# Performance work log

Measured on AMD Instinct MI355X. Metric: run time of the kernel, lower is better.

## Reference

```python
import jax, jax.numpy as jnp
import numpy as np

# ---- model dims (match init_kwargs) ----
BATCH, SEQ, DM = 2, 256, 768
EXPAND, HD, NST = 2, 64, 64
DI = EXPAND * DM            # 1536 d_inner
NH = DI // HD               # 24 heads
R, G = 2, 1                 # mimo_rank, ngroups
SPLIT = NST // 2            # rope_fraction=0.5 -> 32 rotated state dims
NA = SPLIT // 2             # 16 rope angles
AFLOOR, EPS = 1e-4, 1e-5
DINP = 2 * DI + 2 * NST * G * R + 3 * NH + NA  # 3416


def setup_inputs() -> dict:
    key = jax.random.key(0)
    ks = jax.random.split(key, 10)
    def n(k, shp, s=1.0):
        return jax.random.normal(k, shp, jnp.float32) * s
    u = n(ks[0], (BATCH, SEQ, DM))
    in_proj_w = n(ks[1], (DINP, DM), 0.02)
    dt_bias = n(ks[2], (NH,), 0.5)
    B_bias = jnp.ones((NH, R, NST), jnp.float32) + n(ks[3], (NH, R, NST), 0.02)
    C_bias = jnp.ones((NH, R, NST), jnp.float32) + n(ks[4], (NH, R, NST), 0.02)
    B_norm_w = jnp.ones((NST,), jnp.float32)
    C_norm_w = jnp.ones((NST,), jnp.float32)
    mimo_x = jnp.ones((NH, R, HD), jnp.float32) / R + n(ks[5], (NH, R, HD), 0.02)
    mimo_o = jnp.ones((NH, R, HD), jnp.float32) / R + n(ks[6], (NH, R, HD), 0.02)
    D = jnp.ones((NH,), jnp.float32)
    out_proj_w = n(ks[7], (DM, DI), 0.02)
    return dict(u=u, in_proj_w=in_proj_w, dt_bias=dt_bias, B_bias=B_bias,
                C_bias=C_bias, B_norm_w=B_norm_w, C_norm_w=C_norm_w,
                mimo_x=mimo_x, mimo_o=mimo_o, D=D, out_proj_w=out_proj_w)


def _rms(x, w):
    return x * jax.lax.rsqrt(jnp.mean(x * x, -1, keepdims=True) + EPS) * w


def _rope(x, theta):
    # x: (b,l,r,h,n); theta: (b,l,h,NA). Rotate first SPLIT dims in consecutive pairs.
    b, l, r, h, n = x.shape
    xr = x[..., :SPLIT].reshape(b, l, r, h, NA, 2)
    c = jnp.cos(theta)[:, :, None]            # (b,l,1,h,NA)
    s = jnp.sin(theta)[:, :, None]
    x0, x1 = xr[..., 0], xr[..., 1]
    rot = jnp.stack([x0 * c - x1 * s, x0 * s + x1 * c], -1).reshape(b, l, r, h, SPLIT)
    return jnp.concatenate([rot, x[..., SPLIT:]], -1)


def _forward(u, in_proj_w, dt_bias, B_bias, C_bias, B_norm_w, C_norm_w,
             mimo_x, mimo_o, D, out_proj_w):
    b, l, _ = u.shape
    proj = u @ in_proj_w.T                                    # (b,l,DINP)
    sp = np.cumsum([DI, DI, NST * G * R, NST * G * R, NH, NH, NH])
    z, x, Bm, Cm, dd_dt, dd_A, trap, ang = jnp.split(proj, sp, axis=-1)
    z = z.reshape(b, l, NH, HD)
    x = x.reshape(b, l, NH, HD)
    Bm = Bm.reshape(b, l, R, G, NST)[:, :, :, 0]              # g=1 -> (b,l,r,n)
    Cm = Cm.reshape(b, l, R, G, NST)[:, :, :, 0]
    A = jnp.minimum(-jax.nn.softplus(dd_A), -AFLOOR)          # (b,l,h)
    DT = jax.nn.softplus(dd_dt + dt_bias)                     # (b,l,h)
    at = jnp.exp(A * DT)                                      # decay per step
    lam = jax.nn.sigmoid(trap)                                # trapezoid blend
    Bm = _rms(Bm, B_norm_w)
    Cm = _rms(Cm, C_norm_w)
    # per-head multiplicative bias (B_bias/C_bias init to ones -> scale) : (b,l,r,h,n)
    Bh = Bm[:, :, :, None, :] * B_bias.transpose(1, 0, 2)
    Ch = Cm[:, :, :, None, :] * C_bias.transpose(1, 0, 2)
    # data-dependent rotary: cumulative angle theta_t = sum_{s<=t} dt_s * angles_s
    theta = jnp.cumsum(DT[..., None] * ang[:, :, None, :], axis=1)  # (b,l,h,NA)
    Bh = _rope(Bh, theta)
    Ch = _rope(Ch, theta)
    mv = mimo_x.transpose(1, 0, 2)                            # (r,h,p)
    mo = mimo_o.transpose(1, 0, 2)                            # (r,h,p)

    def step(carry, inp):
        S, Bp, vp = carry                                      # S:(b,r,h,p,n)
        Bt, Ct, vt, att, dtt, lamt, zt = inp
        f = jnp.einsum('brhp,brhn->brhpn', vt[:, None] * mv, Bt)
        fp = jnp.einsum('brhp,brhn->brhpn', vp[:, None] * mv, Bp)
        a5 = att[:, None, :, None, None]
        d5 = dtt[:, None, :, None, None]
        l5 = lamt[:, None, :, None, None]
        S = a5 * S + d5 * (l5 * f + (1.0 - l5) * a5 * fp)      # trapezoidal update
        y = jnp.einsum('brhn,brhpn->brhp', Ct, S)
        y = jnp.einsum('brhp,rhp->bhp', y, mo) + D[None, :, None] * vt
        y = y * jax.nn.silu(zt)                                # gated output
        return (S, Bt, vt), y

    S0 = jnp.zeros((b, R, NH, HD, NST), jnp.float32)
    B0 = jnp.zeros((b, R, NH, NST), jnp.float32)
    v0 = jnp.zeros((b, NH, HD), jnp.float32)
    inps = (jnp.moveaxis(Bh, 1, 0), jnp.moveaxis(Ch, 1, 0), jnp.moveaxis(x, 1, 0),
            jnp.moveaxis(at, 1, 0), jnp.moveaxis(DT, 1, 0), jnp.moveaxis(lam, 1, 0),
            jnp.moveaxis(z, 1, 0))
    _, ys = jax.lax.scan(step, (S0, B0, v0), inps)             # ys:(l,b,h,p)
    y = jnp.moveaxis(ys, 0, 1).reshape(b, l, DI)
    return y @ out_proj_w.T                                    # (b,l,DM)


def reference(u, in_proj_w, dt_bias, B_bias, C_bias, B_norm_w, C_norm_w,
              mimo_x, mimo_o, D, out_proj_w):
    return _forward(u, in_proj_w, dt_bias, B_bias, C_bias, B_norm_w, C_norm_w,
                    mimo_x, mimo_o, D, out_proj_w)
```

## Files before the change

kernel.cpp:

```cpp
#include <hip/hip_runtime.h>
#include <hip/hip_bf16.h>
#include <math.h>

typedef __bf16 bf16x8 __attribute__((ext_vector_type(8)));
typedef float  f32x4  __attribute__((ext_vector_type(4)));

#define BATCH 2
#define SEQ   256
#define DMODL 768
#define DIEXP 1536
#define NHEAD 24
#define HDIM  64
#define NSTATE 64
#define RRANK 2
#define NANG  16
#define HALFSPLIT 32
#define DINP  3416
#define DINP_PAD 3456
#define AFLOOR 1e-4f
#define EPSV   1e-5f

__device__ __forceinline__ float softplusf(float x) {
    if (x > 20.f) return x;
    return log1pf(expf(x));
}
__device__ __forceinline__ float sigmoidf_(float x) {
    return 1.f / (1.f + __expf(-x));
}
__device__ __forceinline__ ushort f2bf(float f) {
    uint u = __float_as_uint(f);
    uint r = (u + 0x7FFFu + ((u >> 16) & 1u)) >> 16;
    return (ushort)r;
}
__device__ __forceinline__ float bf2f(ushort x) {
    uint u = ((uint)x) << 16;
    return __uint_as_float(u);
}

__global__ __launch_bounds__(256) void gemm1(const float* __restrict__ A,
        const float* __restrict__ W, ushort* __restrict__ ZT, ushort* __restrict__ XT,
        ushort* __restrict__ BC, float* __restrict__ DTA) {
    const int bm = blockIdx.y * 64, bn = blockIdx.x * 64;
    const int tid = threadIdx.x;
    const int wv = tid >> 6, lane = tid & 63;
    const int wr = (wv >> 1) * 32, wc = (wv & 1) * 32;
    __shared__ ushort As[2][64 * 64];
    __shared__ ushort Bs[2][64 * 64];
    __shared__ ushort Ts[64][72];
    const int srow = tid >> 4, sc4 = tid & 15;
    const int NT = DMODL >> 6;
    float4 ra[4], rw[4];

    auto load_tile = [&](int t) {
        const int k0 = t * 64;
        #pragma unroll
        for (int p = 0; p < 4; ++p)
            ra[p] = *(const float4*)(A + (size_t)(bm + p * 16 + srow) * DMODL + k0 + sc4 * 4);
        #pragma unroll
        for (int p = 0; p < 4; ++p) {
            int r = p * 16 + srow;
            rw[p] = (bn + r < DINP)
                  ? *(const float4*)(W + (size_t)(bn + r) * DMODL + k0 + sc4 * 4)
                  : (float4){0.f, 0.f, 0.f, 0.f};
        }
    };
    auto write_tile = [&](int buf) {
        #pragma unroll
        for (int p = 0; p < 4; ++p) {
            int r = p * 16 + srow;
            int byt = (sc4 * 8) ^ ((r & 7) << 4);
            ushort4 h;
            h.x = f2bf(ra[p].x); h.y = f2bf(ra[p].y);
            h.z = f2bf(ra[p].z); h.w = f2bf(ra[p].w);
            *(ushort4*)(&As[buf][r * 64 + (byt >> 1)]) = h;
        }
        #pragma unroll
        for (int p = 0; p < 4; ++p) {
            int r = p * 16 + srow;
            int byt = (sc4 * 8) ^ ((r & 7) << 4);
            ushort4 h;
            h.x = f2bf(rw[p].x); h.y = f2bf(rw[p].y);
            h.z = f2bf(rw[p].z); h.w = f2bf(rw[p].w);
            *(ushort4*)(&Bs[buf][r * 64 + (byt >> 1)]) = h;
        }
    };

    f32x4 acc[2][2];
    #pragma unroll
    for (int m = 0; m < 2; ++m)
        #pragma unroll
        for (int n = 0; n < 2; ++n) acc[m][n] = (f32x4){0.f, 0.f, 0.f, 0.f};
    const int fr = lane & 15, fk = (lane >> 4) * 16;

    auto compute = [&](int buf) {
        #pragma unroll
        for (int kk = 0; kk < 2; ++kk) {
            bf16x8 af[2], bff[2];
            #pragma unroll
            for (int m = 0; m < 2; ++m) {
                int r = wr + m * 16 + fr;
                int byt = (kk * 64 + fk) ^ ((r & 7) << 4);
                af[m] = *(const bf16x8*)(&As[buf][r * 64 + (byt >> 1)]);
            }
            #pragma unroll
            for (int n = 0; n < 2; ++n) {
                int r = wc + n * 16 + fr;
                int byt = (kk * 64 + fk) ^ ((r & 7) << 4);
                bff[n] = *(const bf16x8*)(&Bs[buf][r * 64 + (byt >> 1)]);
            }
            #pragma unroll
            for (int m = 0; m < 2; ++m)
                #pragma unroll
                for (int n = 0; n < 2; ++n)
                    acc[m][n] = __builtin_amdgcn_mfma_f32_16x16x32_bf16(af[m], bff[n], acc[m][n], 0, 0, 0);
        }
    };

    load_tile(0);
    write_tile(0);
    __syncthreads();
    for (int t = 0; t < NT; ++t) {
        if (t + 1 < NT) load_tile(t + 1);
        compute(t & 1);
        if (t + 1 < NT) write_tile((t + 1) & 1);
        __syncthreads();
    }

    const int r0 = bm + wr + (lane >> 4) * 4;
    if (bn >= 3328) {
        #pragma unroll
        for (int n = 0; n < 2; ++n) {
            int col = bn + wc + n * 16 + fr;
            #pragma unroll
            for (int m = 0; m < 2; ++m)
                #pragma unroll
                for (int r = 0; r < 4; ++r)
                    DTA[(size_t)(col - 3328) * 512 + r0 + m * 16 + r] = acc[m][n][r];
        }
        return;
    }
    #pragma unroll
    for (int m = 0; m < 2; ++m)
        #pragma unroll
        for (int n = 0; n < 2; ++n)
            #pragma unroll
            for (int r = 0; r < 4; ++r)
                Ts[wr + m * 16 + (lane >> 4) * 4 + r][wc + n * 16 + fr] =
                    f2bf(acc[m][n][r]);
    __syncthreads();
    if (bn < 3072) {
        const bool isX = bn >= 1536;
        const int hh = (bn - (isX ? 1536 : 0)) >> 6;
        const int bb = bm >> 8, l0 = bm & 255;
        ushort* dst = (isX ? XT : ZT);
        const int p = tid >> 2, t0 = (tid & 3) * 16;
        ushort* o = dst + ((size_t)(bb * NHEAD + hh) * HDIM + p) * SEQ + l0 + t0;
        #pragma unroll
        for (int k = 0; k < 16; ++k) o[k] = Ts[t0 + k][p];
    } else {
        const int c0 = bn - 3072;
        const int rr = tid >> 2, cs = (tid & 3) * 16;
        ushort* o = BC + (size_t)(bm + rr) * 256 + c0 + cs;
        #pragma unroll
        for (int k = 0; k < 16; ++k) o[k] = Ts[rr][cs + k];
    }
}

__global__ __launch_bounds__(256) void gemm2(const ushort* __restrict__ A,
        const float* __restrict__ W, float* __restrict__ Part) {
    const int bm = blockIdx.y * 64, bn = blockIdx.x * 64, ks = blockIdx.z;
    const int kbase = ks * 384;
    const int tid = threadIdx.x;
    const int wv = tid >> 6, lane = tid & 63;
    const int wr = (wv >> 1) * 32, wc = (wv & 1) * 32;
    __shared__ ushort As[2][64 * 64];
    __shared__ ushort Bs[2][64 * 64];
    const int srow = tid >> 4, sc4 = tid & 15;
    const int arow = tid >> 3, acol = (tid & 7) * 8;
    const int NT = 6;
    uint4 ra[2];
    float4 rw[4];

    auto load_tile = [&](int t) {
        const int k0 = kbase + t * 64;
        #pragma unroll
        for (int p = 0; p < 2; ++p)
            ra[p] = *(const uint4*)(A + (size_t)(bm + p * 32 + arow) * DIEXP + k0 + acol);
        #pragma unroll
        for (int p = 0; p < 4; ++p)
            rw[p] = *(const float4*)(W + (size_t)(bn + p * 16 + srow) * DIEXP + k0 + sc4 * 4);
    };
    auto write_tile = [&](int buf) {
        #pragma unroll
        for (int p = 0; p < 2; ++p) {
            int r = p * 32 + arow;
            int byt = (acol * 2) ^ ((r & 7) << 4);
            *(uint4*)(&As[buf][r * 64 + (byt >> 1)]) = ra[p];
        }
        #pragma unroll
        for (int p = 0; p < 4; ++p) {
            int r = p * 16 + srow;
            int byt = (sc4 * 8) ^ ((r & 7) << 4);
            ushort4 h;
            h.x = f2bf(rw[p].x); h.y = f2bf(rw[p].y);
            h.z = f2bf(rw[p].z); h.w = f2bf(rw[p].w);
            *(ushort4*)(&Bs[buf][r * 64 + (byt >> 1)]) = h;
        }
    };

    f32x4 acc[2][2];
    #pragma unroll
    for (int m = 0; m < 2; ++m)
        #pragma unroll
        for (int n = 0; n < 2; ++n) acc[m][n] = (f32x4){0.f, 0.f, 0.f, 0.f};
    const int fr = lane & 15, fk = (lane >> 4) * 16;

    auto compute = [&](int buf) {
        #pragma unroll
        for (int kk = 0; kk < 2; ++kk) {
            bf16x8 af[2], bff[2];
            #pragma unroll
            for (int m = 0; m < 2; ++m) {
                int r = wr + m * 16 + fr;
                int byt = (kk * 64 + fk) ^ ((r & 7) << 4);
                af[m] = *(const bf16x8*)(&As[buf][r * 64 + (byt >> 1)]);
            }
            #pragma unroll
            for (int n = 0; n < 2; ++n) {
                int r = wc + n * 16 + fr;
                int byt = (kk * 64 + fk) ^ ((r & 7) << 4);
                bff[n] = *(const bf16x8*)(&Bs[buf][r * 64 + (byt >> 1)]);
            }
            #pragma unroll
            for (int m = 0; m < 2; ++m)
                #pragma unroll
                for (int n = 0; n < 2; ++n)
                    acc[m][n] = __builtin_amdgcn_mfma_f32_16x16x32_bf16(af[m], bff[n], acc[m][n], 0, 0, 0);
        }
    };

    load_tile(0);
    write_tile(0);
    __syncthreads();
    for (int t = 0; t < NT; ++t) {
        if (t + 1 < NT) load_tile(t + 1);
        compute(t & 1);
        if (t + 1 < NT) write_tile((t + 1) & 1);
        __syncthreads();
    }

    const int r0 = bm + wr + (lane >> 4) * 4;
    float* P = Part + (size_t)ks * 512 * DMODL;
    #pragma unroll
    for (int n = 0; n < 2; ++n) {
        int col = bn + wc + n * 16 + fr;
        #pragma unroll
        for (int m = 0; m < 2; ++m)
            #pragma unroll
            for (int r = 0; r < 4; ++r)
                P[(size_t)(r0 + m * 16 + r) * DMODL + col] = acc[m][n][r];
    }
}

__global__ void reduce4(const float* __restrict__ Part, float* __restrict__ out) {
    const int i = blockIdx.x * 256 + threadIdx.x;
    const float4* p4 = (const float4*)Part;
    float4 a = p4[i];
    float4 b = p4[i + 98304];
    float4 c = p4[i + 196608];
    float4 d = p4[i + 294912];
    float4 r;
    r.x = a.x + b.x + c.x + d.x;
    r.y = a.y + b.y + c.y + d.y;
    r.z = a.z + b.z + c.z + d.z;
    r.w = a.w + b.w + c.w + d.w;
    ((float4*)out)[i] = r;
}

__global__ __launch_bounds__(256) void scan_kernel(const float* __restrict__ DTA,
        const float* __restrict__ dt_bias, float* __restrict__ DTv,
        float* __restrict__ lamv, float* __restrict__ Pc, float* __restrict__ theta) {
    const int bh = blockIdx.x;
    const int b = bh / NHEAD, h = bh % NHEAD;
    const int tid = threadIdx.x;
    __shared__ float mm[SEQ][18];
    const int l = tid;
    const int gl = b * SEQ + l;
    float DT  = softplusf(DTA[(size_t)h * 512 + gl] + dt_bias[h]);
    float Asp = fmaxf(softplusf(DTA[(size_t)(24 + h) * 512 + gl]), AFLOOR);
    float la  = -Asp * DT;
    float lam = sigmoidf_(DTA[(size_t)(48 + h) * 512 + gl]);
    DTv[bh * SEQ + l] = DT;
    lamv[bh * SEQ + l] = lam;
    #pragma unroll
    for (int i = 0; i < NANG; ++i) mm[l][i] = DT * DTA[(size_t)(72 + i) * 512 + gl];
    mm[l][16] = la;
    __syncthreads();
    const int wv = tid >> 6, lane = tid & 63;
    for (int ch = wv; ch < 17; ch += 4) {
        float carry = 0.f;
        for (int seg = 0; seg < 4; ++seg) {
            float v = mm[seg * 64 + lane][ch];
            #pragma unroll
            for (int off = 1; off < 64; off <<= 1) {
                float t = __shfl_up(v, off);
                if (lane >= off) v += t;
            }
            v += carry;
            carry = __shfl(v, 63);
            int ll = seg * 64 + lane;
            if (ch < 16)
                theta[((size_t)(b * SEQ + ll) * NHEAD + h) * NANG + ch] = v;
            else
                Pc[bh * SEQ + ll] = v;
        }
    }
}

__global__ __launch_bounds__(256) void prep3(const ushort* __restrict__ BC,
        const float* __restrict__ Bbias, const float* __restrict__ Cbias,
        const float* __restrict__ Bnw, const float* __restrict__ Cnw,
        const float* __restrict__ theta,
        ushort* __restrict__ Bh, ushort* __restrict__ Ch) {
    int bl = blockIdx.x;
    int b = bl / SEQ, l = bl % SEQ;
    int tid = threadIdx.x;
    __shared__ float sB[RRANK][NSTATE], sC[RRANK][NSTATE], scale[4];
    __shared__ float thl[NHEAD * NANG];
    const ushort* row = BC + (size_t)bl * 256;
    if (tid < 128) {
        int r = tid / 64, n = tid % 64;
        sB[r][n] = bf2f(row[r * 64 + n]);
    } else {
        int t2 = tid - 128;
        int r = t2 / 64, n = t2 % 64;
        sC[r][n] = bf2f(row[128 + r * 64 + n]);
    }
    for (int k = tid; k < NHEAD * NANG; k += 256)
        thl[k] = theta[(size_t)bl * NHEAD * NANG + k];
    __syncthreads();
    int g = tid / 64, lane = tid % 64;
    float v = (g < 2) ? sB[g][lane] : sC[g - 2][lane];
    float ss = v * v;
    #pragma unroll
    for (int off = 32; off; off >>= 1) ss += __shfl_xor(ss, off);
    if (lane == 0) scale[g] = rsqrtf(ss / NSTATE + EPSV);
    __syncthreads();
    float scB[2] = {scale[0], scale[1]};
    float scC[2] = {scale[2], scale[3]};
    for (int idx = tid; idx < RRANK * NHEAD * NSTATE; idx += 256) {
        int n = idx % NSTATE;
        int h = (idx / NSTATE) % NHEAD;
        int r = idx / (NSTATE * NHEAD);
        float outB, outC;
        if (n < HALFSPLIT) {
            int i = n >> 1;
            int n0 = i * 2, n1 = n0 + 1;
            float th = thl[h * NANG + i];
            float c = cosf(th), s = sinf(th);
            float b0 = sB[r][n0] * scB[r] * Bnw[n0] * Bbias[(h * RRANK + r) * NSTATE + n0];
            float b1 = sB[r][n1] * scB[r] * Bnw[n1] * Bbias[(h * RRANK + r) * NSTATE + n1];
            float c0 = sC[r][n0] * scC[r] * Cnw[n0] * Cbias[(h * RRANK + r) * NSTATE + n0];
            float c1 = sC[r][n1] * scC[r] * Cnw[n1] * Cbias[(h * RRANK + r) * NSTATE + n1];
            outB = (n & 1) ? (b0 * s + b1 * c) : (b0 * c - b1 * s);
            outC = (n & 1) ? (c0 * s + c1 * c) : (c0 * c - c1 * s);
        } else {
            outB = sB[r][n] * scB[r] * Bnw[n] * Bbias[(h * RRANK + r) * NSTATE + n];
            outC = sC[r][n] * scC[r] * Cnw[n] * Cbias[(h * RRANK + r) * NSTATE + n];
        }
        size_t o = ((size_t)((b * RRANK + r) * NHEAD + h) * SEQ + l) * NSTATE + n;
        Bh[o] = f2bf(outB);
        Ch[o] = f2bf(outC);
    }
}

__global__ __launch_bounds__(256) void att2(const ushort* __restrict__ Bh,
        const ushort* __restrict__ Ch, const ushort* __restrict__ XT,
        const ushort* __restrict__ ZT, const float* __restrict__ Pc,
        const float* __restrict__ DTv, const float* __restrict__ lamv,
        const float* __restrict__ mimo_x, const float* __restrict__ mimo_o,
        const float* __restrict__ Dvec, ushort* __restrict__ Yc) {
    const int bh = blockIdx.x, tt = blockIdx.y;
    const int b = bh / NHEAD, h = bh % NHEAD;
    const int tid = threadIdx.x, wv = tid >> 6, lane = tid & 63;
    __shared__ float Pl[SEQ], u1s[SEQ], u2s[SEQ];
    __shared__ ushort Pld[2][4][16][72];
    for (int t = tid; t < SEQ; t += 256) {
        Pl[t]  = Pc[bh * SEQ + t];
        u1s[t] = DTv[bh * SEQ + t] * lamv[bh * SEQ + t];
        u2s[t] = (t + 1 < SEQ) ? DTv[bh * SEQ + t + 1] * (1.f - lamv[bh * SEQ + t + 1]) : 0.f;
    }
    __syncthreads();
    const int r16 = lane & 15, kg = (lane >> 4) * 8;
    const int trow = tt * 64 + wv * 16;
    const int tr0 = trow + (lane >> 4) * 4;
    const int brh0 = (b * RRANK + 0) * NHEAD + h;
    const int brh1 = (b * RRANK + 1) * NHEAD + h;
    bf16x8 ca[2][2];
    {
        const ushort* cp0 = Ch + ((size_t)brh0 * SEQ + trow + r16) * NSTATE + kg;
        const ushort* cp1 = Ch + ((size_t)brh1 * SEQ + trow + r16) * NSTATE + kg;
        ca[0][0] = *(const bf16x8*)cp0;  ca[0][1] = *(const bf16x8*)(cp0 + 32);
        ca[1][0] = *(const bf16x8*)cp1;  ca[1][1] = *(const bf16x8*)(cp1 + 32);
    }
    f32x4 yacc[2][4];
    #pragma unroll
    for (int r2 = 0; r2 < 2; ++r2)
        #pragma unroll
        for (int pf = 0; pf < 4; ++pf) yacc[r2][pf] = (f32x4){0.f, 0.f, 0.f, 0.f};
    float Pt[4];
    #pragma unroll
    for (int r = 0; r < 4; ++r) Pt[r] = Pl[tr0 + r];
    const float Dh = Dvec[h];

    for (int jt = 0; jt <= tt; ++jt) {
        bf16x8 xf[4][2];
        #pragma unroll
        for (int pf = 0; pf < 4; ++pf) {
            const ushort* xp = XT + ((size_t)bh * HDIM + pf * 16 + r16) * SEQ + jt * 64 + kg;
            xf[pf][0] = *(const bf16x8*)xp;
            xf[pf][1] = *(const bf16x8*)(xp + 32);
        }
        f32x4 g[2][4];
        #pragma unroll
        for (int r2 = 0; r2 < 2; ++r2) {
            const size_t bbase = (size_t)(r2 ? brh1 : brh0) * SEQ;
            #pragma unroll
            for (int nf = 0; nf < 4; ++nf) {
                const ushort* bp = Bh + (bbase + jt * 64 + nf * 16 + r16) * NSTATE + kg;
                bf16x8 b0 = *(const bf16x8*)bp;
                bf16x8 b1 = *(const bf16x8*)(bp + 32);
                f32x4 gg = (f32x4){0.f, 0.f, 0.f, 0.f};
                gg = __builtin_amdgcn_mfma_f32_16x16x32_bf16(ca[r2][0], b0, gg, 0, 0, 0);
                gg = __builtin_amdgcn_mfma_f32_16x16x32_bf16(ca[r2][1], b1, gg, 0, 0, 0);
                g[r2][nf] = gg;
            }
        }
        float w[4][4];
        #pragma unroll
        for (int nf = 0; nf < 4; ++nf) {
            const int j = jt * 64 + nf * 16 + r16;
            const float Pj = Pl[j], v1 = u1s[j], v2 = u2s[j];
            #pragma unroll
            for (int r = 0; r < 4; ++r) {
                const int t = tr0 + r;
                w[nf][r] = (j <= t) ? __expf(Pt[r] - Pj) * (v1 + ((j < t) ? v2 : 0.f)) : 0.f;
            }
        }
        #pragma unroll
        for (int r2 = 0; r2 < 2; ++r2)
            #pragma unroll
            for (int nf = 0; nf < 4; ++nf)
                #pragma unroll
                for (int r = 0; r < 4; ++r)
                    Pld[r2][wv][(lane >> 4) * 4 + r][nf * 16 + r16] = f2bf(g[r2][nf][r] * w[nf][r]);
        #pragma unroll
        for (int r2 = 0; r2 < 2; ++r2) {
            bf16x8 pa0 = *(const bf16x8*)&Pld[r2][wv][r16][kg];
            bf16x8 pa1 = *(const bf16x8*)&Pld[r2][wv][r16][32 + kg];
            #pragma unroll
            for (int pf = 0; pf < 4; ++pf) {
                yacc[r2][pf] = __builtin_amdgcn_mfma_f32_16x16x32_bf16(pa0, xf[pf][0], yacc[r2][pf], 0, 0, 0);
                yacc[r2][pf] = __builtin_amdgcn_mfma_f32_16x16x32_bf16(pa1, xf[pf][1], yacc[r2][pf], 0, 0, 0);
            }
        }
    }
    #pragma unroll
    for (int pf = 0; pf < 4; ++pf) {
        const int p = pf * 16 + r16;
        const float mm0 = mimo_x[(h * RRANK + 0) * HDIM + p] * mimo_o[(h * RRANK + 0) * HDIM + p];
        const float mm1 = mimo_x[(h * RRANK + 1) * HDIM + p] * mimo_o[(h * RRANK + 1) * HDIM + p];
        ushort4 xv4 = *(const ushort4*)&XT[((size_t)bh * HDIM + p) * SEQ + tr0];
        ushort4 zv4 = *(const ushort4*)&ZT[((size_t)bh * HDIM + p) * SEQ + tr0];
        const ushort* xvp = (const ushort*)&xv4;
        const ushort* zvp = (const ushort*)&zv4;
        #pragma unroll
        for (int r = 0; r < 4; ++r) {
            const int t = tr0 + r;
            float xv = bf2f(xvp[r]);
            float zv = bf2f(zvp[r]);
            float y = yacc[0][pf][r] * mm0 + yacc[1][pf][r] * mm1 + Dh * xv;
            y *= zv * sigmoidf_(zv);
            Yc[(size_t)(b * SEQ + t) * DIEXP + h * HDIM + p] = f2bf(y);
        }
    }
}

extern "C" void kernel_launch(void* const* d_in, const int* in_sizes, int n_in,
                              void* d_out, int out_size, void* d_ws, size_t ws_size,
                              hipStream_t stream) {
    const float* u        = (const float*)d_in[0];
    const float* in_w     = (const float*)d_in[1];
    const float* dt_bias  = (const float*)d_in[2];
    const float* B_bias   = (const float*)d_in[3];
    const float* C_bias   = (const float*)d_in[4];
    const float* B_norm_w = (const float*)d_in[5];
    const float* C_norm_w = (const float*)d_in[6];
    const float* mimo_x   = (const float*)d_in[7];
    const float* mimo_o   = (const float*)d_in[8];
    const float* Dvec     = (const float*)d_in[9];
    const float* out_w    = (const float*)d_in[10];
    float* out = (float*)d_out;

    float* ws = (float*)d_ws;
    ushort* ZT    = (ushort*)(ws);
    ushort* XT    = (ushort*)(ws + 393216);
    ushort* BC    = (ushort*)(ws + 786432);
    float*  DTA   = ws + 851968;
    ushort* Bh_bf = (ushort*)(ws + 917504);
    ushort* Ch_bf = (ushort*)(ws + 1703936);
    float*  theta = ws + 2490368;
    float*  Pc    = ws + 2686976;
    float*  DTv   = ws + 2699264;
    float*  lamv  = ws + 2711552;
    ushort* Yc_bf = (ushort*)(ws + 2723840);
    float*  Part  = ws + 3117056;

    gemm1<<<dim3(DINP_PAD / 64, 8), 256, 0, stream>>>(u, in_w, ZT, XT, BC, DTA);
    scan_kernel<<<BATCH * NHEAD, 256, 0, stream>>>(DTA, dt_bias, DTv, lamv, Pc, theta);
    prep3<<<BATCH * SEQ, 256, 0, stream>>>(BC, B_bias, C_bias, B_norm_w, C_norm_w,
                                           theta, Bh_bf, Ch_bf);
    att2<<<dim3(BATCH * NHEAD, 4), 256, 0, stream>>>(Bh_bf, Ch_bf, XT, ZT, Pc, DTv,
                                                     lamv, mimo_x, mimo_o, Dvec, Yc_bf);
    gemm2<<<dim3(DMODL / 64, 8, 4), 256, 0, stream>>>(Yc_bf, out_w, Part);
    reduce4<<<384, 256, 0, stream>>>(Part, out);
}
```

Before: 66.34 us.

## Fuse scan with B/C prep and replace split-K reduce with atomics

Merges the cumulative-sum scan kernel and the per-token B/C normalisation+RoPE kernel into one per-(batch,head) kernel that keeps theta in shared memory instead of round-tripping through global memory. That kernel also zeroes the output buffer, so the split-K out-projection GEMM can atomically add into it and the separate partials buffer and reduce kernel are dropped. This removes two launches and the theta and partial-sum traffic. In exchange the prep work is spread over only 48 blocks, float atomics make the summation order nondeterministic, and __sincosf is less accurate than sinf/cosf.

Result: slower. 101.6 us (+53.2%).

```diff
diff --git a/kernel.cpp b/kernel.cpp
--- a/kernel.cpp
+++ b/kernel.cpp
@@ -166,124 +166,23 @@
     }
 }
 
-__global__ __launch_bounds__(256) void gemm2(const ushort* __restrict__ A,
-        const float* __restrict__ W, float* __restrict__ Part) {
-    const int bm = blockIdx.y * 64, bn = blockIdx.x * 64, ks = blockIdx.z;
-    const int kbase = ks * 384;
-    const int tid = threadIdx.x;
-    const int wv = tid >> 6, lane = tid & 63;
-    const int wr = (wv >> 1) * 32, wc = (wv & 1) * 32;
-    __shared__ ushort As[2][64 * 64];
-    __shared__ ushort Bs[2][64 * 64];
-    const int srow = tid >> 4, sc4 = tid & 15;
-    const int arow = tid >> 3, acol = (tid & 7) * 8;
-    const int NT = 6;
-    uint4 ra[2];
-    float4 rw[4];
-
-    auto load_tile = [&](int t) {
-        const int k0 = kbase + t * 64;
-        #pragma unroll
-        for (int p = 0; p < 2; ++p)
-            ra[p] = *(const uint4*)(A + (size_t)(bm + p * 32 + arow) * DIEXP + k0 + acol);
-        #pragma unroll
-        for (int p = 0; p < 4; ++p)
-            rw[p] = *(const float4*)(W + (size_t)(bn + p * 16 + srow) * DIEXP + k0 + sc4 * 4);
-    };
-    auto write_tile = [&](int buf) {
-        #pragma unroll
-        for (int p = 0; p < 2; ++p) {
-            int r = p * 32 + arow;
-            int byt = (acol * 2) ^ ((r & 7) << 4);
-            *(uint4*)(&As[buf][r * 64 + (byt >> 1)]) = ra[p];
-        }
-        #pragma unroll
-        for (int p = 0; p < 4; ++p) {
-            int r = p * 16 + srow;
-            int byt = (sc4 * 8) ^ ((r & 7) << 4);
-            ushort4 h;
-            h.x = f2bf(rw[p].x); h.y = f2bf(rw[p].y);
-            h.z = f2bf(rw[p].z); h.w = f2bf(rw[p].w);
-            *(ushort4*)(&Bs[buf][r * 64 + (byt >> 1)]) = h;
-        }
-    };
-
-    f32x4 acc[2][2];
-    #pragma unroll
-    for (int m = 0; m < 2; ++m)
-        #pragma unroll
-        for (int n = 0; n < 2; ++n) acc[m][n] = (f32x4){0.f, 0.f, 0.f, 0.f};
-    const int fr = lane & 15, fk = (lane >> 4) * 16;
-
-    auto compute = [&](int buf) {
-        #pragma unroll
-        for (int kk = 0; kk < 2; ++kk) {
-            bf16x8 af[2], bff[2];
-            #pragma unroll
-            for (int m = 0; m < 2; ++m) {
-                int r = wr + m * 16 + fr;
-                int byt = (kk * 64 + fk) ^ ((r & 7) << 4);
-                af[m] = *(const bf16x8*)(&As[buf][r * 64 + (byt >> 1)]);
-            }
-            #pragma unroll
-            for (int n = 0; n < 2; ++n) {
-                int r = wc + n * 16 + fr;
-                int byt = (kk * 64 + fk) ^ ((r & 7) << 4);
-                bff[n] = *(const bf16x8*)(&Bs[buf][r * 64 + (byt >> 1)]);
-            }
-            #pragma unroll
-            for (int m = 0; m < 2; ++m)
-                #pragma unroll
-                for (int n = 0; n < 2; ++n)
-                    acc[m][n] = __builtin_amdgcn_mfma_f32_16x16x32_bf16(af[m], bff[n], acc[m][n], 0, 0, 0);
-        }
-    };
-
-    load_tile(0);
-    write_tile(0);
-    __syncthreads();
-    for (int t = 0; t < NT; ++t) {
-        if (t + 1 < NT) load_tile(t + 1);
-        compute(t & 1);
-        if (t + 1 < NT) write_tile((t + 1) & 1);
-        __syncthreads();
-    }
-
-    const int r0 = bm + wr + (lane >> 4) * 4;
-    float* P = Part + (size_t)ks * 512 * DMODL;
-    #pragma unroll
-    for (int n = 0; n < 2; ++n) {
-        int col = bn + wc + n * 16 + fr;
-        #pragma unroll
-        for (int m = 0; m < 2; ++m)
-            #pragma unroll
-            for (int r = 0; r < 4; ++r)
-                P[(size_t)(r0 + m * 16 + r) * DMODL + col] = acc[m][n][r];
-    }
-}
-
-__global__ void reduce4(const float* __restrict__ Part, float* __restrict__ out) {
-    const int i = blockIdx.x * 256 + threadIdx.x;
-    const float4* p4 = (const float4*)Part;
-    float4 a = p4[i];
-    float4 b = p4[i + 98304];
-    float4 c = p4[i + 196608];
-    float4 d = p4[i + 294912];
-    float4 r;
-    r.x = a.x + b.x + c.x + d.x;
-    r.y = a.y + b.y + c.y + d.y;
-    r.z = a.z + b.z + c.z + d.z;
-    r.w = a.w + b.w + c.w + d.w;
-    ((float4*)out)[i] = r;
-}
-
-__global__ __launch_bounds__(256) void scan_kernel(const float* __restrict__ DTA,
-        const float* __restrict__ dt_bias, float* __restrict__ DTv,
-        float* __restrict__ lamv, float* __restrict__ Pc, float* __restrict__ theta) {
+__global__ __launch_bounds__(256) void scanprep(const float* __restrict__ DTA,
+        const ushort* __restrict__ BC, const float* __restrict__ dt_bias,
+        const float* __restrict__ Bbias, const float* __restrict__ Cbias,
+        const float* __restrict__ Bnw, const float* __restrict__ Cnw,
+        float* __restrict__ DTv, float* __restrict__ lamv, float* __restrict__ Pc,
+        ushort* __restrict__ Bh, ushort* __restrict__ Ch, float* __restrict__ outZ) {
     const int bh = blockIdx.x;
     const int b = bh / NHEAD, h = bh % NHEAD;
     const int tid = threadIdx.x;
+    {
+        float4* o4 = (float4*)outZ;
+        int base = bh * 2048 + tid;
+        #pragma unroll
+        for (int k = 0; k < 8; ++k) o4[base + k * 256] = (float4){0.f, 0.f, 0.f, 0.f};
+    }
     __shared__ float mm[SEQ][18];
+    __shared__ float thl[SEQ][NANG];
     const int l = tid;
     const int gl = b * SEQ + l;
     float DT  = softplusf(DTA[(size_t)h * 512 + gl] + dt_bias[h]);
@@ -310,67 +209,57 @@
             carry = __shfl(v, 63);
             int ll = seg * 64 + lane;
             if (ch < 16)
-                theta[((size_t)(b * SEQ + ll) * NHEAD + h) * NANG + ch] = v;
+                thl[ll][ch] = v;
             else
                 Pc[bh * SEQ + ll] = v;
         }
     }
-}
-
-__global__ __launch_bounds__(256) void prep3(const ushort* __restrict__ BC,
-        const float* __restrict__ Bbias, const float* __restrict__ Cbias,
-        const float* __restrict__ Bnw, const float* __restrict__ Cnw,
-        const float* __restrict__ theta,
-        ushort* __restrict__ Bh, ushort* __restrict__ Ch) {
-    int bl = blockIdx.x;
-    int b = bl / SEQ, l = bl % SEQ;
-    int tid = threadIdx.x;
-    __shared__ float sB[RRANK][NSTATE], sC[RRANK][NSTATE], scale[4];
-    __shared__ float thl[NHEAD * NANG];
-    const ushort* row = BC + (size_t)bl * 256;
-    if (tid < 128) {
-        int r = tid / 64, n = tid % 64;
-        sB[r][n] = bf2f(row[r * 64 + n]);
-    } else {
-        int t2 = tid - 128;
-        int r = t2 / 64, n = t2 % 64;
-        sC[r][n] = bf2f(row[128 + r * 64 + n]);
-    }
-    for (int k = tid; k < NHEAD * NANG; k += 256)
-        thl[k] = theta[(size_t)bl * NHEAD * NANG + k];
     __syncthreads();
-    int g = tid / 64, lane = tid % 64;
-    float v = (g < 2) ? sB[g][lane] : sC[g - 2][lane];
-    float ss = v * v;
-    #pragma unroll
-    for (int off = 32; off; off >>= 1) ss += __shfl_xor(ss, off);
-    if (lane == 0) scale[g] = rsqrtf(ss / NSTATE + EPSV);
-    __syncthreads();
-    float scB[2] = {scale[0], scale[1]};
-    float scC[2] = {scale[2], scale[3]};
-    for (int idx = tid; idx < RRANK * NHEAD * NSTATE; idx += 256) {
-        int n = idx % NSTATE;
-        int h = (idx / NSTATE) % NHEAD;
-        int r = idx / (NSTATE * NHEAD);
-        float outB, outC;
+    const int n = lane;
+    const float bw  = Bnw[n], cw = Cnw[n];
+    const float bb0 = Bbias[(h * RRANK + 0) * NSTATE + n];
+    const float bb1 = Bbias[(h * RRANK + 1) * NSTATE + n];
+    const float cb0 = Cbias[(h * RRANK + 0) * NSTATE + n];
+    const float cb1 = Cbias[(h * RRANK + 1) * NSTATE + n];
+    for (int ll = wv; ll < SEQ; ll += 4) {
+        const ushort* row = BC + (size_t)(b * SEQ + ll) * 256;
+        float vB0 = bf2f(row[n]);
+        float vB1 = bf2f(row[64 + n]);
+        float vC0 = bf2f(row[128 + n]);
+        float vC1 = bf2f(row[192 + n]);
+        float s0 = vB0 * vB0, s1 = vB1 * vB1, s2 = vC0 * vC0, s3 = vC1 * vC1;
+        #pragma unroll
+        for (int off = 32; off; off >>= 1) {
+            s0 += __shfl_xor(s0, off); s1 += __shfl_xor(s1, off);
+            s2 += __shfl_xor(s2, off); s3 += __shfl_xor(s3, off);
+        }
+        float b0 = vB0 * rsqrtf(s0 / 64.f + EPSV) * bw * bb0;
+        float b1 = vB1 * rsqrtf(s1 / 64.f + EPSV) * bw * bb1;
+        float c0 = vC0 * rsqrtf(s2 / 64.f + EPSV) * cw * cb0;
+        float c1 = vC1 * rsqrtf(s3 / 64.f + EPSV) * cw * cb1;
+        float pB0 = __shfl_xor(b0, 1), pB1 = __shfl_xor(b1, 1);
+        float pC0 = __shfl_xor(c0, 1), pC1 = __shfl_xor(c1, 1);
+        float outB0 = b0, outB1 = b1, outC0 = c0, outC1 = c1;
         if (n < HALFSPLIT) {
-            int i = n >> 1;
-            int n0 = i * 2, n1 = n0 + 1;
-            float th = thl[h * NANG + i];
-            float c = cosf(th), s = sinf(th);
-            float b0 = sB[r][n0] * scB[r] * Bnw[n0] * Bbias[(h * RRANK + r) * NSTATE + n0];
-            float b1 = sB[r][n1] * scB[r] * Bnw[n1] * Bbias[(h * RRANK + r) * NSTATE + n1];
-            float c0 = sC[r][n0] * scC[r] * Cnw[n0] * Cbias[(h * RRANK + r) * NSTATE + n0];
-            float c1 = sC[r][n1] * scC[r] * Cnw[n1] * Cbias[(h * RRANK + r) * NSTATE + n1];
-            outB = (n & 1) ? (b0 * s + b1 * c) : (b0 * c - b1 * s);
-            outC = (n & 1) ? (c0 * s + c1 * c) : (c0 * c - c1 * s);
-        } else {
-            outB = sB[r][n] * scB[r] * Bnw[n] * Bbias[(h * RRANK + r) * NSTATE + n];
-            outC = sC[r][n] * scC[r] * Cnw[n] * Cbias[(h * RRANK + r) * NSTATE + n];
-        }
-        size_t o = ((size_t)((b * RRANK + r) * NHEAD + h) * SEQ + l) * NSTATE + n;
-        Bh[o] = f2bf(outB);
-        Ch[o] = f2bf(outC);
+            float th = thl[ll][n >> 1];
+            float sth, cth;
+            __sincosf(th, &sth, &cth);
+            if ((n & 1) == 0) {
+                outB0 = b0 * cth - pB0 * sth;
+                outB1 = b1 * cth - pB1 * sth;
+                outC0 = c0 * cth - pC0 * sth;
+                outC1 = c1 * cth - pC1 * sth;
+            } else {
+                outB0 = pB0 * sth + b0 * cth;
+                outB1 = pB1 * sth + b1 * cth;
+                outC0 = pC0 * sth + c0 * cth;
+                outC1 = pC1 * sth + c1 * cth;
+            }
+        }
+        size_t o0 = ((size_t)((b * RRANK + 0) * NHEAD + h) * SEQ + ll) * NSTATE + n;
+        size_t o1 = ((size_t)((b * RRANK + 1) * NHEAD + h) * SEQ + ll) * NSTATE + n;
+        Bh[o0] = f2bf(outB0);  Bh[o1] = f2bf(outB1);
+        Ch[o0] = f2bf(outC0);  Ch[o1] = f2bf(outC1);
     }
 }
 
@@ -486,6 +375,101 @@
     }
 }
 
+__global__ __launch_bounds__(256) void gemm2(const ushort* __restrict__ A,
+        const float* __restrict__ W, float* __restrict__ out) {
+    const int bm = blockIdx.y * 64, bn = blockIdx.x * 64, ks = blockIdx.z;
+    const int kbase = ks * 384;
+    const int tid = threadIdx.x;
+    const int wv = tid >> 6, lane = tid & 63;
+    const int wr = (wv >> 1) * 32, wc = (wv & 1) * 32;
+    __shared__ ushort As[2][64 * 64];
+    __shared__ ushort Bs[2][64 * 64];
+    const int srow = tid >> 4, sc4 = tid & 15;
+    const int arow = tid >> 3, acol = (tid & 7) * 8;
+    const int NT = 6;
+    uint4 ra[2];
+    float4 rw[4];
+
+    auto load_tile = [&](int t) {
+        const int k0 = kbase + t * 64;
+        #pragma unroll
+        for (int p = 0; p < 2; ++p)
+            ra[p] = *(const uint4*)(A + (size_t)(bm + p * 32 + arow) * DIEXP + k0 + acol);
+        #pragma unroll
+        for (int p = 0; p < 4; ++p)
+            rw[p] = *(const float4*)(W + (size_t)(bn + p * 16 + srow) * DIEXP + k0 + sc4 * 4);
+    };
+    auto write_tile = [&](int buf) {
+        #pragma unroll
+        for (int p = 0; p < 2; ++p) {
+            int r = p * 32 + arow;
+            int byt = (acol * 2) ^ ((r & 7) << 4);
+            *(uint4*)(&As[buf][r * 64 + (byt >> 1)]) = ra[p];
+        }
+        #pragma unroll
+        for (int p = 0; p < 4; ++p) {
+            int r = p * 16 + srow;
+            int byt = (sc4 * 8) ^ ((r & 7) << 4);
+            ushort4 h;
+            h.x = f2bf(rw[p].x); h.y = f2bf(rw[p].y);
+            h.z = f2bf(rw[p].z); h.w = f2bf(rw[p].w);
+            *(ushort4*)(&Bs[buf][r * 64 + (byt >> 1)]) = h;
+        }
+    };
+
+    f32x4 acc[2][2];
+    #pragma unroll
+    for (int m = 0; m < 2; ++m)
+        #pragma unroll
+        for (int n = 0; n < 2; ++n) acc[m][n] = (f32x4){0.f, 0.f, 0.f, 0.f};
+    const int fr = lane & 15, fk = (lane >> 4) * 16;
+
+    auto compute = [&](int buf) {
+        #pragma unroll
+        for (int kk = 0; kk < 2; ++kk) {
+            bf16x8 af[2], bff[2];
+            #pragma unroll
+            for (int m = 0; m < 2; ++m) {
+                int r = wr + m * 16 + fr;
+                int byt = (kk * 64 + fk) ^ ((r & 7) << 4);
+                af[m] = *(const bf16x8*)(&As[buf][r * 64 + (byt >> 1)]);
+            }
+            #pragma unroll
+            for (int n = 0; n < 2; ++n) {
+                int r = wc + n * 16 + fr;
+                int byt = (kk * 64 + fk) ^ ((r & 7) << 4);
+                bff[n] = *(const bf16x8*)(&Bs[buf][r * 64 + (byt >> 1)]);
+            }
+            #pragma unroll
+            for (int m = 0; m < 2; ++m)
+                #pragma unroll
+                for (int n = 0; n < 2; ++n)
+                    acc[m][n] = __builtin_amdgcn_mfma_f32_16x16x32_bf16(af[m], bff[n], acc[m][n], 0, 0, 0);
+        }
+    };
+
+    load_tile(0);
+    write_tile(0);
+    __syncthreads();
+    for (int t = 0; t < NT; ++t) {
+        if (t + 1 < NT) load_tile(t + 1);
+        compute(t & 1);
+        if (t + 1 < NT) write_tile((t + 1) & 1);
+        __syncthreads();
+    }
+
+    const int r0 = bm + wr + (lane >> 4) * 4;
+    #pragma unroll
+    for (int n = 0; n < 2; ++n) {
+        int col = bn + wc + n * 16 + fr;
+        #pragma unroll
+        for (int m = 0; m < 2; ++m)
+            #pragma unroll
+            for (int r = 0; r < 4; ++r)
+                atomicAdd(&out[(size_t)(r0 + m * 16 + r) * DMODL + col], acc[m][n][r]);
+    }
+}
+
 extern "C" void kernel_launch(void* const* d_in, const int* in_sizes, int n_in,
                               void* d_out, int out_size, void* d_ws, size_t ws_size,
                               hipStream_t stream) {
@@ -509,19 +493,16 @@
     float*  DTA   = ws + 851968;
     ushort* Bh_bf = (ushort*)(ws + 917504);
     ushort* Ch_bf = (ushort*)(ws + 1703936);
-    float*  theta = ws + 2490368;
-    float*  Pc    = ws + 2686976;
-    float*  DTv   = ws + 2699264;
-    float*  lamv  = ws + 2711552;
-    ushort* Yc_bf = (ushort*)(ws + 2723840);
-    float*  Part  = ws + 3117056;
+    float*  Pc    = ws + 2490368;
+    float*  DTv   = ws + 2502656;
+    float*  lamv  = ws + 2514944;
+    ushort* Yc_bf = (ushort*)(ws + 2527232);
 
     gemm1<<<dim3(DINP_PAD / 64, 8), 256, 0, stream>>>(u, in_w, ZT, XT, BC, DTA);
-    scan_kernel<<<BATCH * NHEAD, 256, 0, stream>>>(DTA, dt_bias, DTv, lamv, Pc, theta);
-    prep3<<<BATCH * SEQ, 256, 0, stream>>>(BC, B_bias, C_bias, B_norm_w, C_norm_w,
-                                           theta, Bh_bf, Ch_bf);
+    scanprep<<<BATCH * NHEAD, 256, 0, stream>>>(DTA, BC, dt_bias, B_bias, C_bias,
+                                                B_norm_w, C_norm_w, DTv, lamv, Pc,
+                                                Bh_bf, Ch_bf, out);
     att2<<<dim3(BATCH * NHEAD, 4), 256, 0, stream>>>(Bh_bf, Ch_bf, XT, ZT, Pc, DTv,
                                                      lamv, mimo_x, mimo_o, Dvec, Yc_bf);
-    gemm2<<<dim3(DMODL / 64, 8, 4), 256, 0, stream>>>(Yc_bf, out_w, Part);
-    reduce4<<<384, 256, 0, stream>>>(Part, out);
-}
+    gemm2<<<dim3(DMODL / 64, 8, 4), 256, 0, stream>>>(Yc_bf, out_w, out);
+}
```

## Replace split-K partial buffer and reduce kernel with atomic accumulation into output

Applied to the files above, without the earlier changes.

The out-projection GEMM now atomically adds its four split-K partial results straight into the output instead of writing partials to workspace and launching a separate reduce kernel. The output is zeroed inside the scan kernel, which runs earlier in the stream, so no extra launch is needed. Separately, the rope cos/sin in prep3 now use the fast __sincosf intrinsic. This removes one launch and the round trip through the partial buffer. In exchange it adds atomic contention, a nondeterministic summation order and slightly lower sincos accuracy.

New measurement: 64.98 us, median of 2. -2.0%, faster.

```diff
diff --git a/kernel.cpp b/kernel.cpp
--- a/kernel.cpp
+++ b/kernel.cpp
@@ -166,123 +166,19 @@
     }
 }
 
-__global__ __launch_bounds__(256) void gemm2(const ushort* __restrict__ A,
-        const float* __restrict__ W, float* __restrict__ Part) {
-    const int bm = blockIdx.y * 64, bn = blockIdx.x * 64, ks = blockIdx.z;
-    const int kbase = ks * 384;
-    const int tid = threadIdx.x;
-    const int wv = tid >> 6, lane = tid & 63;
-    const int wr = (wv >> 1) * 32, wc = (wv & 1) * 32;
-    __shared__ ushort As[2][64 * 64];
-    __shared__ ushort Bs[2][64 * 64];
-    const int srow = tid >> 4, sc4 = tid & 15;
-    const int arow = tid >> 3, acol = (tid & 7) * 8;
-    const int NT = 6;
-    uint4 ra[2];
-    float4 rw[4];
-
-    auto load_tile = [&](int t) {
-        const int k0 = kbase + t * 64;
-        #pragma unroll
-        for (int p = 0; p < 2; ++p)
-            ra[p] = *(const uint4*)(A + (size_t)(bm + p * 32 + arow) * DIEXP + k0 + acol);
-        #pragma unroll
-        for (int p = 0; p < 4; ++p)
-            rw[p] = *(const float4*)(W + (size_t)(bn + p * 16 + srow) * DIEXP + k0 + sc4 * 4);
-    };
-    auto write_tile = [&](int buf) {
-        #pragma unroll
-        for (int p = 0; p < 2; ++p) {
-            int r = p * 32 + arow;
-            int byt = (acol * 2) ^ ((r & 7) << 4);
-            *(uint4*)(&As[buf][r * 64 + (byt >> 1)]) = ra[p];
-        }
-        #pragma unroll
-        for (int p = 0; p < 4; ++p) {
-            int r = p * 16 + srow;
-            int byt = (sc4 * 8) ^ ((r & 7) << 4);
-            ushort4 h;
-            h.x = f2bf(rw[p].x); h.y = f2bf(rw[p].y);
-            h.z = f2bf(rw[p].z); h.w = f2bf(rw[p].w);
-            *(ushort4*)(&Bs[buf][r * 64 + (byt >> 1)]) = h;
-        }
-    };
-
-    f32x4 acc[2][2];
-    #pragma unroll
-    for (int m = 0; m < 2; ++m)
-        #pragma unroll
-        for (int n = 0; n < 2; ++n) acc[m][n] = (f32x4){0.f, 0.f, 0.f, 0.f};
-    const int fr = lane & 15, fk = (lane >> 4) * 16;
-
-    auto compute = [&](int buf) {
-        #pragma unroll
-        for (int kk = 0; kk < 2; ++kk) {
-            bf16x8 af[2], bff[2];
-            #pragma unroll
-            for (int m = 0; m < 2; ++m) {
-                int r = wr + m * 16 + fr;
-                int byt = (kk * 64 + fk) ^ ((r & 7) << 4);
-                af[m] = *(const bf16x8*)(&As[buf][r * 64 + (byt >> 1)]);
-            }
-            #pragma unroll
-            for (int n = 0; n < 2; ++n) {
-                int r = wc + n * 16 + fr;
-                int byt = (kk * 64 + fk) ^ ((r & 7) << 4);
-                bff[n] = *(const bf16x8*)(&Bs[buf][r * 64 + (byt >> 1)]);
-            }
-            #pragma unroll
-            for (int m = 0; m < 2; ++m)
-                #pragma unroll
-                for (int n = 0; n < 2; ++n)
-                    acc[m][n] = __builtin_amdgcn_mfma_f32_16x16x32_bf16(af[m], bff[n], acc[m][n], 0, 0, 0);
-        }
-    };
-
-    load_tile(0);
-    write_tile(0);
-    __syncthreads();
-    for (int t = 0; t < NT; ++t) {
-        if (t + 1 < NT) load_tile(t + 1);
-        compute(t & 1);
-        if (t + 1 < NT) write_tile((t + 1) & 1);
-        __syncthreads();
-    }
-
-    const int r0 = bm + wr + (lane >> 4) * 4;
-    float* P = Part + (size_t)ks * 512 * DMODL;
-    #pragma unroll
-    for (int n = 0; n < 2; ++n) {
-        int col = bn + wc + n * 16 + fr;
-        #pragma unroll
-        for (int m = 0; m < 2; ++m)
-            #pragma unroll
-            for (int r = 0; r < 4; ++r)
-                P[(size_t)(r0 + m * 16 + r) * DMODL + col] = acc[m][n][r];
-    }
-}
-
-__global__ void reduce4(const float* __restrict__ Part, float* __restrict__ out) {
-    const int i = blockIdx.x * 256 + threadIdx.x;
-    const float4* p4 = (const float4*)Part;
-    float4 a = p4[i];
-    float4 b = p4[i + 98304];
-    float4 c = p4[i + 196608];
-    float4 d = p4[i + 294912];
-    float4 r;
-    r.x = a.x + b.x + c.x + d.x;
-    r.y = a.y + b.y + c.y + d.y;
-    r.z = a.z + b.z + c.z + d.z;
-    r.w = a.w + b.w + c.w + d.w;
-    ((float4*)out)[i] = r;
-}
-
 __global__ __launch_bounds__(256) void scan_kernel(const float* __restrict__ DTA,
         const float* __restrict__ dt_bias, float* __restrict__ DTv,
-        float* __restrict__ lamv, float* __restrict__ Pc, float* __restrict__ theta) {
+        float* __restrict__ lamv, float* __restrict__ Pc, float* __restrict__ theta,
+        float* __restrict__ outZ) {
     const int bh = blockIdx.x;
     const int b = bh / NHEAD, h = bh % NHEAD;
     const int tid = threadIdx.x;
+    {
+        float4* o4 = (float4*)outZ;
+        int base = bh * 2048 + tid;
+        #pragma unroll
+        for (int k = 0; k < 8; ++k) o4[base + k * 256] = (float4){0.f, 0.f, 0.f, 0.f};
+    }
     __shared__ float mm[SEQ][18];
     const int l = tid;
     const int gl = b * SEQ + l;
@@ -357,7 +253,8 @@
             int i = n >> 1;
             int n0 = i * 2, n1 = n0 + 1;
             float th = thl[h * NANG + i];
-            float c = cosf(th), s = sinf(th);
+            float c, s;
+            __sincosf(th, &s, &c);
             float b0 = sB[r][n0] * scB[r] * Bnw[n0] * Bbias[(h * RRANK + r) * NSTATE + n0];
             float b1 = sB[r][n1] * scB[r] * Bnw[n1] * Bbias[(h * RRANK + r) * NSTATE + n1];
             float c0 = sC[r][n0] * scC[r] * Cnw[n0] * Cbias[(h * RRANK + r) * NSTATE + n0];
@@ -486,6 +383,101 @@
     }
 }
 
+__global__ __launch_bounds__(256) void gemm2(const ushort* __restrict__ A,
+        const float* __restrict__ W, float* __restrict__ out) {
+    const int bm = blockIdx.y * 64, bn = blockIdx.x * 64, ks = blockIdx.z;
+    const int kbase = ks * 384;
+    const int tid = threadIdx.x;
+    const int wv = tid >> 6, lane = tid & 63;
+    const int wr = (wv >> 1) * 32, wc = (wv & 1) * 32;
+    __shared__ ushort As[2][64 * 64];
+    __shared__ ushort Bs[2][64 * 64];
+    const int srow = tid >> 4, sc4 = tid & 15;
+    const int arow = tid >> 3, acol = (tid & 7) * 8;
+    const int NT = 6;
+    uint4 ra[2];
+    float4 rw[4];
+
+    auto load_tile = [&](int t) {
+        const int k0 = kbase + t * 64;
+        #pragma unroll
+        for (int p = 0; p < 2; ++p)
+            ra[p] = *(const uint4*)(A + (size_t)(bm + p * 32 + arow) * DIEXP + k0 + acol);
+        #pragma unroll
+        for (int p = 0; p < 4; ++p)
+            rw[p] = *(const float4*)(W + (size_t)(bn + p * 16 + srow) * DIEXP + k0 + sc4 * 4);
+    };
+    auto write_tile = [&](int buf) {
+        #pragma unroll
+        for (int p = 0; p < 2; ++p) {
+            int r = p * 32 + arow;
+            int byt = (acol * 2) ^ ((r & 7) << 4);
+            *(uint4*)(&As[buf][r * 64 + (byt >> 1)]) = ra[p];
+        }
+        #pragma unroll
+        for (int p = 0; p < 4; ++p) {
+            int r = p * 16 + srow;
+            int byt = (sc4 * 8) ^ ((r & 7) << 4);
+            ushort4 h;
+            h.x = f2bf(rw[p].x); h.y = f2bf(rw[p].y);
+            h.z = f2bf(rw[p].z); h.w = f2bf(rw[p].w);
+            *(ushort4*)(&Bs[buf][r * 64 + (byt >> 1)]) = h;
+        }
+    };
+
+    f32x4 acc[2][2];
+    #pragma unroll
+    for (int m = 0; m < 2; ++m)
+        #pragma unroll
+        for (int n = 0; n < 2; ++n) acc[m][n] = (f32x4){0.f, 0.f, 0.f, 0.f};
+    const int fr = lane & 15, fk = (lane >> 4) * 16;
+
+    auto compute = [&](int buf) {
+        #pragma unroll
+        for (int kk = 0; kk < 2; ++kk) {
+            bf16x8 af[2], bff[2];
+            #pragma unroll
+            for (int m = 0; m < 2; ++m) {
+                int r = wr + m * 16 + fr;
+                int byt = (kk * 64 + fk) ^ ((r & 7) << 4);
+                af[m] = *(const bf16x8*)(&As[buf][r * 64 + (byt >> 1)]);
+            }
+            #pragma unroll
+            for (int n = 0; n < 2; ++n) {
+                int r = wc + n * 16 + fr;
+                int byt = (kk * 64 + fk) ^ ((r & 7) << 4);
+                bff[n] = *(const bf16x8*)(&Bs[buf][r * 64 + (byt >> 1)]);
+            }
+            #pragma unroll
+            for (int m = 0; m < 2; ++m)
+                #pragma unroll
+                for (int n = 0; n < 2; ++n)
+                    acc[m][n] = __builtin_amdgcn_mfma_f32_16x16x32_bf16(af[m], bff[n], acc[m][n], 0, 0, 0);
+        }
+    };
+
+    load_tile(0);
+    write_tile(0);
+    __syncthreads();
+    for (int t = 0; t < NT; ++t) {
+        if (t + 1 < NT) load_tile(t + 1);
+        compute(t & 1);
+        if (t + 1 < NT) write_tile((t + 1) & 1);
+        __syncthreads();
+    }
+
+    const int r0 = bm + wr + (lane >> 4) * 4;
+    #pragma unroll
+    for (int n = 0; n < 2; ++n) {
+        int col = bn + wc + n * 16 + fr;
+        #pragma unroll
+        for (int m = 0; m < 2; ++m)
+            #pragma unroll
+            for (int r = 0; r < 4; ++r)
+                atomicAdd(&out[(size_t)(r0 + m * 16 + r) * DMODL + col], acc[m][n][r]);
+    }
+}
+
 extern "C" void kernel_launch(void* const* d_in, const int* in_sizes, int n_in,
                               void* d_out, int out_size, void* d_ws, size_t ws_size,
                               hipStream_t stream) {
@@ -514,14 +506,13 @@
     float*  DTv   = ws + 2699264;
     float*  lamv  = ws + 2711552;
     ushort* Yc_bf = (ushort*)(ws + 2723840);
-    float*  Part  = ws + 3117056;
 
     gemm1<<<dim3(DINP_PAD / 64, 8), 256, 0, stream>>>(u, in_w, ZT, XT, BC, DTA);
-    scan_kernel<<<BATCH * NHEAD, 256, 0, stream>>>(DTA, dt_bias, DTv, lamv, Pc, theta);
+    scan_kernel<<<BATCH * NHEAD, 256, 0, stream>>>(DTA, dt_bias, DTv, lamv, Pc,
+                                                   theta, out);
     prep3<<<BATCH * SEQ, 256, 0, stream>>>(BC, B_bias, C_bias, B_norm_w, C_norm_w,
                                            theta, Bh_bf, Ch_bf);
     att2<<<dim3(BATCH * NHEAD, 4), 256, 0, stream>>>(Bh_bf, Ch_bf, XT, ZT, Pc, DTv,
                                                      lamv, mimo_x, mimo_o, Dvec, Yc_bf);
-    gemm2<<<dim3(DMODL / 64, 8, 4), 256, 0, stream>>>(Yc_bf, out_w, Part);
-    reduce4<<<384, 256, 0, stream>>>(Part, out);
-}
+    gemm2<<<dim3(DMODL / 64, 8, 4), 256, 0, stream>>>(Yc_bf, out_w, out);
+}
```
